# Kernel tuning notes

Measured on AMD Instinct MI355X. Metric: run time of the kernel, lower is better.

Reference implementation:

```python
import jax, jax.numpy as jnp
import numpy as np

B, T, C = 2, 2048, 1024
H = 16
D = C // H  # head_dim = 64
ROPE_BASE = 10000.0


def _rope_tables(seq_len, dim, dtype=jnp.float32):
    inv_freq = 1.0 / (ROPE_BASE ** (jnp.arange(0, dim, 2, dtype=jnp.float32) / dim))
    t = jnp.arange(seq_len, dtype=jnp.float32)
    freqs = jnp.einsum('i,j->ij', t, inv_freq)          # [T, D/2]
    emb = jnp.concatenate([freqs, freqs], axis=-1)      # [T, D]
    return jnp.cos(emb).astype(dtype), jnp.sin(emb).astype(dtype)


def _rotate_half(x):
    x1, x2 = jnp.split(x, 2, axis=-1)
    return jnp.concatenate([-x2, x1], axis=-1)


def setup_inputs() -> dict:
    key = jax.random.key(0)
    ks = jax.random.split(key, 9)
    s = 0.02
    return {
        'x': jax.random.normal(ks[0], (B, T, C), jnp.float32),
        'Wq': jax.random.normal(ks[1], (C, C), jnp.float32) * s,
        'bq': jax.random.normal(ks[2], (C,), jnp.float32) * s,
        'Wk': jax.random.normal(ks[3], (C, C), jnp.float32) * s,
        'bk': jax.random.normal(ks[4], (C,), jnp.float32) * s,
        'Wv': jax.random.normal(ks[5], (C, C), jnp.float32) * s,
        'bv': jax.random.normal(ks[6], (C,), jnp.float32) * s,
        'Wo': jax.random.normal(ks[7], (C, C), jnp.float32) * s,
        'bo': jax.random.normal(ks[8], (C,), jnp.float32) * s,
    }


def reference(x, Wq, bq, Wk, bk, Wv, bv, Wo, bo):
    b, t, c = x.shape
    q = x @ Wq.T + bq
    k = x @ Wk.T + bk
    v = x @ Wv.T + bv
    # [B, H, T, D]
    q = q.reshape(b, t, H, D).transpose(0, 2, 1, 3)
    k = k.reshape(b, t, H, D).transpose(0, 2, 1, 3)
    v = v.reshape(b, t, H, D).transpose(0, 2, 1, 3)
    cos, sin = _rope_tables(t, D, x.dtype)  # [T, D]
    q = q * cos + _rotate_half(q) * sin
    k = k * cos + _rotate_half(k) * sin
    scale = 1.0 / jnp.sqrt(jnp.array(D, x.dtype))
    scores = jnp.einsum('bhqd,bhkd->bhqk', q, k) * scale
    causal = jnp.triu(jnp.full((t, t), -jnp.inf, dtype=x.dtype), k=1)
    scores = scores + causal
    attn = jax.nn.softmax(scores, axis=-1)
    out = jnp.einsum('bhqk,bhkd->bhqd', attn, v)
    out = out.transpose(0, 2, 1, 3).reshape(b, t, c)
    return out @ Wo.T + bo
```

## Files before the change

kernel.cpp:

```cpp
#include <hip/hip_runtime.h>


typedef unsigned short u16;
typedef unsigned int u32;
typedef __bf16 bf16_t;
typedef bf16_t bf16x8 __attribute__((ext_vector_type(8)));
typedef float f32x4 __attribute__((ext_vector_type(4)));
typedef float f32x16 __attribute__((ext_vector_type(16)));

#if __has_builtin(__builtin_amdgcn_exp2f)
#define EXP2(x) __builtin_amdgcn_exp2f(x)
#else
#define EXP2(x) exp2f(x)
#endif

__device__ __forceinline__ u16 f2bf(float f) {
  union { float f; unsigned u; } v; v.f = f;
  return (u16)((v.u + 0x7FFFu + ((v.u >> 16) & 1u)) >> 16);
}

__device__ __forceinline__ void gload_lds16(const void* g, void* l) {
  __builtin_amdgcn_global_load_lds(
      (const __attribute__((address_space(1))) void*)g,
      (__attribute__((address_space(3))) void*)l, 16, 0, 0);
}

__global__ __launch_bounds__(256) void prep_kernel(
    const float* __restrict__ x, const float* __restrict__ Wq,
    const float* __restrict__ Wk, const float* __restrict__ Wv,
    const float* __restrict__ Wo, const float* __restrict__ bq,
    const float* __restrict__ bk, const float* __restrict__ bv,
    u16* __restrict__ xb, u16* __restrict__ Wqkvo, float* __restrict__ tab,
    float* __restrict__ bcat) {
  const int bid = blockIdx.x, tid = threadIdx.x;
  if (bid < 4096) {
    int i = bid * 256 + tid;
    float4 f = ((const float4*)x)[i];
    ushort4 o;
    o.x = f2bf(f.x); o.y = f2bf(f.y); o.z = f2bf(f.z); o.w = f2bf(f.w);
    ((ushort4*)xb)[i] = o;
  } else if (bid < 8192) {
    int wsel = (bid - 4096) >> 10;
    int i = ((bid - 4096) & 1023) * 256 + tid;
    const float* in = (wsel == 0) ? Wq : (wsel == 1) ? Wk : (wsel == 2) ? Wv : Wo;
    float4 f = ((const float4*)in)[i];
    ushort4 o;
    o.x = f2bf(f.x); o.y = f2bf(f.y); o.z = f2bf(f.z); o.w = f2bf(f.w);
    ((ushort4*)(Wqkvo + (size_t)wsel * 1048576))[i] = o;
  } else if (bid < 8448) {
    int idx = (bid - 8192) * 256 + tid;
    int t = idx >> 5, i = idx & 31;
    float freq = powf(10000.0f, -(float)i * (1.0f / 32.0f));
    float a = (float)t * freq;
    tab[t * 64 + i] = cosf(a);
    tab[t * 64 + 32 + i] = sinf(a);
  } else {
    int j = (bid - 8448) * 256 + tid;
    float v = (j < 1024) ? bq[j] : (j < 2048) ? bk[j - 1024] : bv[j - 2048];
    bcat[j] = v;
  }
}

__device__ __forceinline__ void stage256(const u16* __restrict__ A,
                                         const u16* __restrict__ Bt,
                                         int m0, int n0, int k0,
                                         u16* lA, u16* lB, int tid) {
#pragma unroll
  for (int r = 0; r < 4; ++r) {
    int ch = r * 512 + tid;
    int row = ch >> 3, s = ch & 7;
    gload_lds16(A + (size_t)(m0 + row) * 1024 + k0 + ((s ^ (row & 7)) << 3),
                lA + ch * 8);
  }
#pragma unroll
  for (int r = 0; r < 4; ++r) {
    int ch = r * 512 + tid;
    int row = ch >> 3, s = ch & 7;
    gload_lds16(Bt + (size_t)(n0 + row) * 1024 + k0 + ((s ^ (row & 7)) << 3),
                lB + ch * 8);
  }
}

__device__ __forceinline__ void gemm256_db(const u16* __restrict__ A,
                                           const u16* __restrict__ Bt,
                                           int m0, int n0, u16* lA, u16* lB,
                                           f32x4 acc[8][4]) {
  const int tid = threadIdx.x;
  const int l = tid & 63;
  const int wid = tid >> 6, wr = wid >> 2, wc = wid & 3;

#pragma unroll
  for (int m = 0; m < 8; ++m)
#pragma unroll
    for (int n = 0; n < 4; ++n)
      acc[m][n] = (f32x4){0.f, 0.f, 0.f, 0.f};

  stage256(A, Bt, m0, n0, 0, lA, lB, tid);

  int cur = 0;
  for (int t = 0; t < 16; ++t) {
    if (t + 1 < 16) {
      stage256(A, Bt, m0, n0, (t + 1) * 64, lA + (cur ^ 1) * 16384,
               lB + (cur ^ 1) * 16384, tid);
      asm volatile("s_waitcnt vmcnt(8)" ::: "memory");
    } else {
      asm volatile("s_waitcnt vmcnt(0)" ::: "memory");
    }
    __builtin_amdgcn_s_barrier();

    const u16* pA = lA + cur * 16384;
    const u16* pB = lB + cur * 16384;
#pragma unroll
    for (int kk = 0; kk < 2; ++kk) {
      bf16x8 af[8], bf[4];
#pragma unroll
      for (int m = 0; m < 8; ++m) {
        int row = wr * 128 + m * 16 + (l & 15);
        int slot = (kk * 4 + (l >> 4)) ^ (row & 7);
        af[m] = *(const bf16x8*)(pA + row * 64 + slot * 8);
      }
#pragma unroll
      for (int n = 0; n < 4; ++n) {
        int row = wc * 64 + n * 16 + (l & 15);
        int slot = (kk * 4 + (l >> 4)) ^ (row & 7);
        bf[n] = *(const bf16x8*)(pB + row * 64 + slot * 8);
      }
#pragma unroll
      for (int m = 0; m < 8; ++m)
#pragma unroll
        for (int n = 0; n < 4; ++n)
          acc[m][n] =
              __builtin_amdgcn_mfma_f32_16x16x32_bf16(af[m], bf[n], acc[m][n], 0, 0, 0);
    }
    __builtin_amdgcn_s_barrier();
    cur ^= 1;
  }
}

__global__ __launch_bounds__(512, 2) void qkv_kernel(
    const u16* __restrict__ xb, const u16* __restrict__ Wqkv,
    const float* __restrict__ bcat, const float* __restrict__ tab,
    u16* __restrict__ Q, u16* __restrict__ Kr, u16* __restrict__ Vt) {
  __shared__ __align__(16) u16 lds[65536];
  const int m0 = blockIdx.y * 256, n0 = blockIdx.x * 256;

  f32x4 acc[8][4];
  gemm256_db(xb, Wqkv, m0, n0, lds, lds + 32768, acc);

  const int tid = threadIdx.x, l = tid & 63;
  const int wid = tid >> 6, wr = wid >> 2, wc = wid & 3;
  const int gcb = n0 + wc * 64;
  const int z = gcb >> 10, h = (gcb >> 6) & 15;
  const int grb = m0 + wr * 128;
  const int b2 = grb >> 11, t0 = grb & 2047;
  u16* myl = lds + wid * 8192;

  if (z < 2) {
#pragma unroll
    for (int m = 0; m < 8; ++m)
#pragma unroll
      for (int n = 0; n < 4; ++n)
#pragma unroll
        for (int jr = 0; jr < 4; ++jr) {
          int tl = m * 16 + ((l >> 4) << 2) + jr;
          int d = n * 16 + (l & 15);
          int t = t0 + tl;
          float val = acc[m][n][jr] + bcat[gcb + d];
          float p = acc[m][n ^ 2][jr] + bcat[gcb + (d ^ 32)];
          float cs = tab[t * 64 + (d & 31)];
          float sn = tab[t * 64 + 32 + (d & 31)];
          float rot = (d < 32) ? -p : p;
          float o = val * cs + rot * sn;
          if (z == 0) o *= 0.18033688011112042f;
          myl[tl * 64 + d] = f2bf(o);
        }
    asm volatile("s_waitcnt lgkmcnt(0)" ::: "memory");
    u16* dstb = ((z == 0) ? Q : Kr) + (((size_t)(b2 * 16 + h) << 11) + t0) * 64;
#pragma unroll
    for (int i = 0; i < 16; ++i) {
      int c = i * 64 + l;
      *(bf16x8*)(dstb + c * 8) = *(const bf16x8*)(myl + c * 8);
    }
  } else {
#pragma unroll
    for (int m = 0; m < 8; ++m)
#pragma unroll
      for (int n = 0; n < 4; ++n)
#pragma unroll
        for (int jr = 0; jr < 4; ++jr) {
          int tl = m * 16 + ((l >> 4) << 2) + jr;
          int d = n * 16 + (l & 15);
          float val = acc[m][n][jr] + bcat[gcb + d];
          myl[d * 128 + (tl ^ ((d & 7) << 4))] = f2bf(val);
        }
    asm volatile("s_waitcnt lgkmcnt(0)" ::: "memory");
#pragma unroll
    for (int i = 0; i < 16; ++i) {
      int c = i * 64 + l;
      int d = c >> 4, off = (c & 15) * 8;
      bf16x8 v = *(const bf16x8*)(myl + d * 128 + (off ^ ((d & 7) << 4)));
      *(bf16x8*)(Vt + (((size_t)((b2 * 16 + h) * 64 + d)) << 11) + t0 + off) = v;
    }
  }
}

__global__ __launch_bounds__(512, 2) void outproj_kernel(
    const u16* __restrict__ attn, const u16* __restrict__ Wob,
    const float* __restrict__ bo, float* __restrict__ out) {
  __shared__ __align__(16) u16 lds[65536];
  const int m0 = blockIdx.y * 256, n0 = blockIdx.x * 256;
  f32x4 acc[8][4];
  gemm256_db(attn, Wob, m0, n0, lds, lds + 32768, acc);
  const int tid = threadIdx.x, l = tid & 63;
  const int wid = tid >> 6, wr = wid >> 2, wc = wid & 3;
#pragma unroll
  for (int m = 0; m < 8; ++m)
#pragma unroll
    for (int n = 0; n < 4; ++n)
#pragma unroll
      for (int jr = 0; jr < 4; ++jr) {
        int gr = m0 + wr * 128 + m * 16 + ((l >> 4) << 2) + jr;
        int gc = n0 + wc * 64 + n * 16 + (l & 15);
        out[(size_t)gr * 1024 + gc] = acc[m][n][jr] + bo[gc];
      }
}

__global__ __launch_bounds__(512) void attn_kernel(const u16* __restrict__ Q,
                                                   const u16* __restrict__ K,
                                                   const u16* __restrict__ Vt,
                                                   u16* __restrict__ out) {
  __shared__ __align__(16) u16 lK[2][2][4096];
  __shared__ __align__(16) u16 lV[2][2][4096];
  const int tid = threadIdx.x, l = tid & 63;
  const int w8 = tid >> 6;
  const int grp = w8 >> 2, w = w8 & 3;
  const int gtid = tid & 255;
  const int n = blockIdx.x;
  const int xcd = n & 7, j = n >> 3;
  const int bh = xcd * 4 + (j & 3);
  const int ji = j >> 2;
  const int qb = (ji < 8) ? (15 - ji) : (ji - 8);
  const int b = bh >> 4, h = bh & 15;
  const int lq = l & 31, hl = l >> 5;
  const int q0w = qb * 128 + w * 32;
  const int qg = q0w + lq;

  const u16* qbase = Q + ((((size_t)bh) << 11) + qg) * 64 + hl * 8;
  bf16x8 qf[4];
#pragma unroll
  for (int kd = 0; kd < 4; ++kd) qf[kd] = *(const bf16x8*)(qbase + kd * 16);

  const f32x16 z16 = {0.f, 0.f, 0.f, 0.f, 0.f, 0.f, 0.f, 0.f,
                      0.f, 0.f, 0.f, 0.f, 0.f, 0.f, 0.f, 0.f};
  f32x16 oacc[2];
  oacc[0] = z16; oacc[1] = z16;
  float mi = -1e30f, li = 0.f;

  const int nth = qb + 1;
  const int tb = grp * nth;

#define STAGE_KV(it_, buf_)                                                        \
  {                                                                                \
    _Pragma("unroll") for (int r = 0; r < 2; ++r) {                                \
      int ch = r * 256 + gtid;                                                     \
      int row = ch >> 3, s = ch & 7;                                               \
      gload_lds16(                                                                 \
          K + ((((size_t)bh) << 11) + (it_) * 64 + row) * 64 + ((s ^ (row & 7)) << 3), \
          &lK[grp][buf_][0] + ch * 8);                                             \
    }                                                                              \
    _Pragma("unroll") for (int r = 0; r < 2; ++r) {                                \
      int ch = r * 256 + gtid;                                                     \
      int row = ch >> 3, s = ch & 7;                                               \
      gload_lds16(                                                                 \
          Vt + ((((size_t)bh) * 64 + row) << 11) + (it_) * 64 + ((s ^ (row & 7)) << 3), \
          &lV[grp][buf_][0] + ch * 8);                                             \
    }                                                                              \
  }

  STAGE_KV(tb, 0);
  int cur = 0;

  for (int it = 0; it < nth; ++it) {
    const int tile = tb + it;
    const int kv0 = tile * 64;
    if (it + 1 < nth) {
      STAGE_KV(tile + 1, cur ^ 1);
      asm volatile("s_waitcnt vmcnt(4)" ::: "memory");
    } else {
      asm volatile("s_waitcnt vmcnt(0)" ::: "memory");
    }
    __builtin_amdgcn_s_barrier();

    const bool active = (kv0 <= q0w + 31);
    if (active) {
      const u16* pK = &lK[grp][cur][0];
      const u16* pV = &lV[grp][cur][0];

      f32x16 sacc[2];
      sacc[0] = z16; sacc[1] = z16;
#pragma unroll
      for (int g = 0; g < 2; ++g) {
        int row = g * 32 + lq;
        int sw = row & 7;
#pragma unroll
        for (int kd = 0; kd < 4; ++kd) {
          bf16x8 kf = *(const bf16x8*)(pK + row * 64 + (((kd * 2 + hl) ^ sw) << 3));
          sacc[g] = __builtin_amdgcn_mfma_f32_32x32x16_bf16(kf, qf[kd], sacc[g], 0, 0, 0);
        }
      }

      if (kv0 + 63 > q0w) {
#pragma unroll
        for (int g = 0; g < 2; ++g)
#pragma unroll
          for (int r = 0; r < 16; ++r) {
            int kv = kv0 + g * 32 + (r & 3) + ((r >> 2) << 3) + hl * 4;
            if (kv > qg) sacc[g][r] = -1e30f;
          }
      }

      float mx[16];
#pragma unroll
      for (int r = 0; r < 16; ++r) mx[r] = fmaxf(sacc[0][r], sacc[1][r]);
#pragma unroll
      for (int s = 8; s > 0; s >>= 1)
#pragma unroll
        for (int r = 0; r < s; ++r) mx[r] = fmaxf(mx[r], mx[r + s]);
      float mt = fmaxf(mx[0], __shfl_xor(mx[0], 32, 64));

      if (!__all(mt <= mi + 8.0f)) {
        float mn = fmaxf(mi, mt);
        float al = EXP2(mi - mn);
        mi = mn;
#pragma unroll
        for (int dblk = 0; dblk < 2; ++dblk)
#pragma unroll
          for (int r = 0; r < 16; ++r) oacc[dblk][r] *= al;
        li *= al;
      }
#pragma unroll
      for (int g = 0; g < 2; ++g)
#pragma unroll
        for (int r = 0; r < 16; ++r) sacc[g][r] = EXP2(sacc[g][r] - mi);
      float sm[16];
#pragma unroll
      for (int r = 0; r < 16; ++r) sm[r] = sacc[0][r] + sacc[1][r];
#pragma unroll
      for (int s = 8; s > 0; s >>= 1)
#pragma unroll
        for (int r = 0; r < s; ++r) sm[r] += sm[r + s];
      float rs = sm[0] + __shfl_xor(sm[0], 32, 64);
      li += rs;

      u32 pw[2][8], px[2][8];
#pragma unroll
      for (int g = 0; g < 2; ++g)
#pragma unroll
        for (int i = 0; i < 8; ++i) {
          union { bf16_t h2[2]; u32 u; } pk;
          pk.h2[0] = (bf16_t)sacc[g][2 * i];
          pk.h2[1] = (bf16_t)sacc[g][2 * i + 1];
          pw[g][i] = pk.u;
        }
#pragma unroll
      for (int g = 0; g < 2; ++g)
#pragma unroll
        for (int i = 0; i < 8; ++i)
          px[g][i] = (u32)__shfl_xor((int)pw[g][i], 32, 64);

      bf16x8 pfrag[4];
#pragma unroll
      for (int km = 0; km < 4; ++km) {
        const int g = km >> 1, o = (km & 1) * 4;
        union { u32 u[4]; bf16x8 v; } f;
        f.u[0] = hl ? px[g][o + 2] : pw[g][o + 0];
        f.u[1] = hl ? px[g][o + 3] : pw[g][o + 1];
        f.u[2] = hl ? pw[g][o + 2] : px[g][o + 0];
        f.u[3] = hl ? pw[g][o + 3] : px[g][o + 1];
        pfrag[km] = f.v;
      }

#pragma unroll
      for (int dblk = 0; dblk < 2; ++dblk) {
        int row = dblk * 32 + lq;
        int sw = row & 7;
#pragma unroll
        for (int km = 0; km < 4; ++km) {
          bf16x8 vf = *(const bf16x8*)(pV + row * 64 + (((km * 2 + hl) ^ sw) << 3));
          oacc[dblk] = __builtin_amdgcn_mfma_f32_32x32x16_bf16(vf, pfrag[km],
                                                              oacc[dblk], 0, 0, 0);
        }
      }
    }
    __builtin_amdgcn_s_barrier();
    cur ^= 1;
  }
#undef STAGE_KV

  float* cb = (float*)&lK[0][0][0];
  float* ml = (float*)&lV[0][0][0];
  if (grp == 1) {
    float* myo = cb + w * 2048;
#pragma unroll
    for (int dblk = 0; dblk < 2; ++dblk)
#pragma unroll
      for (int r = 0; r < 16; ++r) {
        int d = dblk * 32 + (r & 3) + ((r >> 2) << 3) + hl * 4;
        myo[d * 32 + lq] = oacc[dblk][r];
      }
    ml[w * 64 + lq] = mi;
    ml[w * 64 + 32 + lq] = li;
  }
  asm volatile("s_waitcnt lgkmcnt(0)" ::: "memory");
  __builtin_amdgcn_s_barrier();

  if (grp == 0) {
    const float m1 = ml[w * 64 + lq];
    const float l1 = ml[w * 64 + 32 + lq];
    const float* po = cb + w * 2048;
    const float m = fmaxf(mi, m1);
    const float w0 = EXP2(mi - m), w1 = EXP2(m1 - m);
    const float inv = 1.0f / (li * w0 + l1 * w1);
    const size_t rowbase = ((size_t)(b * 2048 + qg)) * 1024 + h * 64;
#pragma unroll
    for (int dblk = 0; dblk < 2; ++dblk)
#pragma unroll
      for (int g4 = 0; g4 < 4; ++g4) {
        ushort4 st;
#pragma unroll
        for (int jj = 0; jj < 4; ++jj) {
          int r = g4 * 4 + jj;
          int d = dblk * 32 + g4 * 8 + hl * 4 + jj;
          float o = (oacc[dblk][r] * w0 + po[d * 32 + lq] * w1) * inv;
          ((u16*)&st)[jj] = f2bf(o);
        }
        *(ushort4*)((u16*)out + rowbase + dblk * 32 + g4 * 8 + hl * 4) = st;
      }
  }
}

extern "C" void kernel_launch(void* const* d_in, const int* in_sizes, int n_in,
                              void* d_out, int out_size, void* d_ws, size_t ws_size,
                              hipStream_t stream) {
  const float* x  = (const float*)d_in[0];
  const float* Wq = (const float*)d_in[1];
  const float* bq = (const float*)d_in[2];
  const float* Wk = (const float*)d_in[3];
  const float* bk = (const float*)d_in[4];
  const float* Wv = (const float*)d_in[5];
  const float* bv = (const float*)d_in[6];
  const float* Wo = (const float*)d_in[7];
  const float* bo = (const float*)d_in[8];
  float* out = (float*)d_out;

  char* ws = (char*)d_ws;
  u16* xb    = (u16*)(ws);
  u16* Wqkvo = (u16*)(ws + (8ull << 20));
  u16* Wob   = Wqkvo + 3 * 1048576;
  u16* Qr  = (u16*)(ws + (16ull << 20));
  u16* Kr  = (u16*)(ws + (24ull << 20));
  u16* Vt  = (u16*)(ws + (32ull << 20));
  u16* At  = (u16*)(ws + (40ull << 20));
  float* tab  = (float*)(ws + (48ull << 20));
  float* bcat = (float*)(ws + (48ull << 20) + (512ull << 10));

  prep_kernel<<<dim3(8460), dim3(256), 0, stream>>>(x, Wq, Wk, Wv, Wo, bq, bk, bv,
                                                    xb, Wqkvo, tab, bcat);
  qkv_kernel<<<dim3(12, 16), dim3(512), 0, stream>>>(xb, Wqkvo, bcat, tab,
                                                     Qr, Kr, Vt);
  attn_kernel<<<dim3(512), dim3(512), 0, stream>>>(Qr, Kr, Vt, At);
  outproj_kernel<<<dim3(4, 16), dim3(512), 0, stream>>>(At, Wob, bo, out);
}
```

Measured before the change: 129.8 us.

## Restructure attention to small blocks loading K/V directly into registers

The attention kernel changes from 512-thread blocks that stage K/V tiles through swizzled, double-buffered LDS into 128-thread blocks of two waves, each handling 32 query rows. Each wave reads its K and V fragments straight from global memory into registers and prefetches the next K tile while it computes. The two waves split the KV range in half and merge their partial results through a small LDS buffer. This drops the LDS staging and the per-tile barriers and gives a larger grid for better load balance, but each wave now fetches K/V on its own with no sharing inside the block, so global and L2 traffic goes up and V loads are not overlapped.

```diff
diff --git a/kernel.cpp b/kernel.cpp
--- a/kernel.cpp
+++ b/kernel.cpp
@@ -225,25 +225,25 @@
       }
 }
 
-__global__ __launch_bounds__(512) void attn_kernel(const u16* __restrict__ Q,
+__global__ __launch_bounds__(128) void attn_kernel(const u16* __restrict__ Q,
                                                    const u16* __restrict__ K,
                                                    const u16* __restrict__ Vt,
                                                    u16* __restrict__ out) {
-  __shared__ __align__(16) u16 lK[2][2][4096];
-  __shared__ __align__(16) u16 lV[2][2][4096];
-  const int tid = threadIdx.x, l = tid & 63;
-  const int w8 = tid >> 6;
-  const int grp = w8 >> 2, w = w8 & 3;
-  const int gtid = tid & 255;
+  __shared__ __align__(16) float sO[64 * 32];
+  __shared__ float sML[64];
+  const int tid = threadIdx.x, l = tid & 63, w = tid >> 6;
   const int n = blockIdx.x;
-  const int xcd = n & 7, j = n >> 3;
-  const int bh = xcd * 4 + (j & 3);
-  const int ji = j >> 2;
-  const int qb = (ji < 8) ? (15 - ji) : (ji - 8);
+  const int bh = (n & 7) * 4 + ((n >> 3) & 3);
+  const int qj = 63 - (n >> 5);
   const int b = bh >> 4, h = bh & 15;
   const int lq = l & 31, hl = l >> 5;
-  const int q0w = qb * 128 + w * 32;
+  const int q0w = qj * 32;
   const int qg = q0w + lq;
+  const int nt = (qj >> 1) + 1;
+  const int nh = (nt + 1) >> 1;
+
+  const u16* Kb = K + (((size_t)bh) << 17);
+  const u16* Vb = Vt + (((size_t)bh) << 17);
 
   const u16* qbase = Q + ((((size_t)bh) << 11) + qg) * 64 + hl * 8;
   bf16x8 qf[4];
@@ -256,59 +256,50 @@
   oacc[0] = z16; oacc[1] = z16;
   float mi = -1e30f, li = 0.f;
 
-  const int nth = qb + 1;
-  const int tb = grp * nth;
-
-#define STAGE_KV(it_, buf_)                                                        \
-  {                                                                                \
-    _Pragma("unroll") for (int r = 0; r < 2; ++r) {                                \
-      int ch = r * 256 + gtid;                                                     \
-      int row = ch >> 3, s = ch & 7;                                               \
-      gload_lds16(                                                                 \
-          K + ((((size_t)bh) << 11) + (it_) * 64 + row) * 64 + ((s ^ (row & 7)) << 3), \
-          &lK[grp][buf_][0] + ch * 8);                                             \
-    }                                                                              \
-    _Pragma("unroll") for (int r = 0; r < 2; ++r) {                                \
-      int ch = r * 256 + gtid;                                                     \
-      int row = ch >> 3, s = ch & 7;                                               \
-      gload_lds16(                                                                 \
-          Vt + ((((size_t)bh) * 64 + row) << 11) + (it_) * 64 + ((s ^ (row & 7)) << 3), \
-          &lV[grp][buf_][0] + ch * 8);                                             \
-    }                                                                              \
-  }
-
-  STAGE_KV(tb, 0);
-  int cur = 0;
-
-  for (int it = 0; it < nth; ++it) {
-    const int tile = tb + it;
+  bf16x8 kc[2][4];
+  {
+    const int kv0 = (w ? nh : 0) * 64;
+#pragma unroll
+    for (int g2 = 0; g2 < 2; ++g2)
+#pragma unroll
+      for (int kd = 0; kd < 4; ++kd)
+        kc[g2][kd] = *(const bf16x8*)(Kb + (size_t)(kv0 + g2 * 32 + lq) * 64 +
+                                      kd * 16 + hl * 8);
+  }
+
+  for (int it = 0; it < nh; ++it) {
+    const int tile = w ? nh + it : it;
     const int kv0 = tile * 64;
-    if (it + 1 < nth) {
-      STAGE_KV(tile + 1, cur ^ 1);
-      asm volatile("s_waitcnt vmcnt(4)" ::: "memory");
-    } else {
-      asm volatile("s_waitcnt vmcnt(0)" ::: "memory");
-    }
-    __builtin_amdgcn_s_barrier();
-
-    const bool active = (kv0 <= q0w + 31);
+    const bool active = tile < nt;
+
+    bf16x8 vv[2][4];
+#pragma unroll
+    for (int dblk = 0; dblk < 2; ++dblk)
+#pragma unroll
+      for (int km = 0; km < 4; ++km)
+        vv[dblk][km] = *(const bf16x8*)(Vb + (((size_t)(dblk * 32 + lq)) << 11) +
+                                        kv0 + km * 16 + hl * 8);
+
+    f32x16 sacc[2];
+    sacc[0] = z16; sacc[1] = z16;
+#pragma unroll
+    for (int g2 = 0; g2 < 2; ++g2)
+#pragma unroll
+      for (int kd = 0; kd < 4; ++kd)
+        sacc[g2] = __builtin_amdgcn_mfma_f32_32x32x16_bf16(kc[g2][kd], qf[kd],
+                                                           sacc[g2], 0, 0, 0);
+
+    if (it + 1 < nh) {
+      const int kvn = (tile + 1) * 64;
+#pragma unroll
+      for (int g2 = 0; g2 < 2; ++g2)
+#pragma unroll
+        for (int kd = 0; kd < 4; ++kd)
+          kc[g2][kd] = *(const bf16x8*)(Kb + (size_t)(kvn + g2 * 32 + lq) * 64 +
+                                        kd * 16 + hl * 8);
+    }
+
     if (active) {
-      const u16* pK = &lK[grp][cur][0];
-      const u16* pV = &lV[grp][cur][0];
-
-      f32x16 sacc[2];
-      sacc[0] = z16; sacc[1] = z16;
-#pragma unroll
-      for (int g = 0; g < 2; ++g) {
-        int row = g * 32 + lq;
-        int sw = row & 7;
-#pragma unroll
-        for (int kd = 0; kd < 4; ++kd) {
-          bf16x8 kf = *(const bf16x8*)(pK + row * 64 + (((kd * 2 + hl) ^ sw) << 3));
-          sacc[g] = __builtin_amdgcn_mfma_f32_32x32x16_bf16(kf, qf[kd], sacc[g], 0, 0, 0);
-        }
-      }
-
       if (kv0 + 63 > q0w) {
 #pragma unroll
         for (int g = 0; g < 2; ++g)
@@ -381,43 +372,32 @@
       }
 
 #pragma unroll
-      for (int dblk = 0; dblk < 2; ++dblk) {
-        int row = dblk * 32 + lq;
-        int sw = row & 7;
-#pragma unroll
-        for (int km = 0; km < 4; ++km) {
-          bf16x8 vf = *(const bf16x8*)(pV + row * 64 + (((km * 2 + hl) ^ sw) << 3));
-          oacc[dblk] = __builtin_amdgcn_mfma_f32_32x32x16_bf16(vf, pfrag[km],
-                                                              oacc[dblk], 0, 0, 0);
-        }
-      }
-    }
-    __builtin_amdgcn_s_barrier();
-    cur ^= 1;
-  }
-#undef STAGE_KV
-
-  float* cb = (float*)&lK[0][0][0];
-  float* ml = (float*)&lV[0][0][0];
-  if (grp == 1) {
-    float* myo = cb + w * 2048;
+      for (int dblk = 0; dblk < 2; ++dblk)
+#pragma unroll
+        for (int km = 0; km < 4; ++km)
+          oacc[dblk] = __builtin_amdgcn_mfma_f32_32x32x16_bf16(
+              vv[dblk][km], pfrag[km], oacc[dblk], 0, 0, 0);
+    }
+  }
+
+  if (w == 1) {
 #pragma unroll
     for (int dblk = 0; dblk < 2; ++dblk)
 #pragma unroll
       for (int r = 0; r < 16; ++r) {
         int d = dblk * 32 + (r & 3) + ((r >> 2) << 3) + hl * 4;
-        myo[d * 32 + lq] = oacc[dblk][r];
-      }
-    ml[w * 64 + lq] = mi;
-    ml[w * 64 + 32 + lq] = li;
-  }
-  asm volatile("s_waitcnt lgkmcnt(0)" ::: "memory");
-  __builtin_amdgcn_s_barrier();
-
-  if (grp == 0) {
-    const float m1 = ml[w * 64 + lq];
-    const float l1 = ml[w * 64 + 32 + lq];
-    const float* po = cb + w * 2048;
+        sO[d * 32 + lq] = oacc[dblk][r];
+      }
+    if (hl == 0) {
+      sML[lq] = mi;
+      sML[32 + lq] = li;
+    }
+  }
+  __syncthreads();
+
+  if (w == 0) {
+    const float m1 = sML[lq];
+    const float l1 = sML[32 + lq];
     const float m = fmaxf(mi, m1);
     const float w0 = EXP2(mi - m), w1 = EXP2(m1 - m);
     const float inv = 1.0f / (li * w0 + l1 * w1);
@@ -431,7 +411,7 @@
         for (int jj = 0; jj < 4; ++jj) {
           int r = g4 * 4 + jj;
           int d = dblk * 32 + g4 * 8 + hl * 4 + jj;
-          float o = (oacc[dblk][r] * w0 + po[d * 32 + lq] * w1) * inv;
+          float o = (oacc[dblk][r] * w0 + sO[d * 32 + lq] * w1) * inv;
           ((u16*)&st)[jj] = f2bf(o);
         }
         *(ushort4*)((u16*)out + rowbase + dblk * 32 + g4 * 8 + hl * 4) = st;
@@ -468,6 +448,6 @@
                                                     xb, Wqkvo, tab, bcat);
   qkv_kernel<<<dim3(12, 16), dim3(512), 0, stream>>>(xb, Wqkvo, bcat, tab,
                                                      Qr, Kr, Vt);
-  attn_kernel<<<dim3(512), dim3(512), 0, stream>>>(Qr, Kr, Vt, At);
+  attn_kernel<<<dim3(2048), dim3(128), 0, stream>>>(Qr, Kr, Vt, At);
   outproj_kernel<<<dim3(4, 16), dim3(512), 0, stream>>>(At, Wob, bo, out);
 }
```

After: 149.5 us. +15.2%, slower.
